# Optimization experiments

Hardware: AMD Instinct MI355X
Metric: run time of the kernel (lower is better)

## Reference

```python
import jax, jax.numpy as jnp
import numpy as np

F, C, H, W = 16, 256, 64, 64
N, M = 4096, 8192


def setup_inputs() -> dict:
    key = jax.random.key(0)
    k1, k2, k3, k4, k5 = jax.random.split(key, 5)
    proj_mats = jax.random.normal(k1, (F, 3, 3), dtype=jnp.float32)
    feats = jax.random.normal(k2, (F, C, H, W), dtype=jnp.float32)
    feat_img = jax.random.randint(k3, (N, 1), 0, F, dtype=jnp.int32)
    feat_loc = jax.random.uniform(k4, (N, 2), dtype=jnp.float32) * 64.0
    # tracks: [2, M] matched feature pairs, smaller index first (code contract).
    pair = jax.random.randint(k5, (2, M), 0, N, dtype=jnp.int32)
    tracks = jnp.sort(pair, axis=0)
    return {"proj_mats": proj_mats, "feats": feats, "feat_img": feat_img,
            "feat_loc": feat_loc, "tracks": tracks, "n_img": F}


def _association(tracks, n, n_img):
    """Faithful translation of find_3d_point_association +
    associate_3d_point_indices_2_features. The torch code raises a sparse
    symmetric adjacency (with identity diagonal) to the n_img-th power and
    uses only its NONZERO PATTERN. We use binary exponentiation with
    saturation (min(.,1)), which preserves the nonzero pattern exactly
    (all values are non-negative) while keeping values bounded."""
    A = jnp.zeros((n, n), dtype=jnp.float32)
    A = A.at[tracks[0], tracks[1]].set(1.0)
    A = A.at[tracks[1], tracks[0]].set(1.0)
    d = jnp.arange(n)
    A = A.at[d, d].set(1.0)  # identity diagonal, as in the torch code

    # T = pattern(A ** n_img) via binary exponentiation (n_img is a Python int)
    R, P, e = None, A, int(n_img)
    while e:
        if e & 1:
            R = P if R is None else jnp.minimum(R @ P, 1.0)
        e >>= 1
        if e:
            P = jnp.minimum(P @ P, 1.0)
    T = R

    # leading[j] = min{ i : T[i,j] != 0, i <= j }  (diag guarantees j itself)
    rows = d[:, None]
    cand = jnp.where((T > 0) & (rows <= d[None, :]), rows, n)
    leading = cand.min(axis=0)  # [N] int32

    # self-leading features get consecutive 3D-point ids in index order;
    # everyone else inherits the id of its (self-leading) leading feature.
    is_self = leading == d
    point_id = jnp.cumsum(is_self.astype(jnp.int32)) - 1  # rank among self-leading
    association = point_id[leading]
    return association


def reference(proj_mats, feats, feat_img, feat_loc, tracks, n_img):
    n = feat_img.shape[0]
    association = _association(tracks, n, n_img)
    return association
```

## Files before the change

kernel.cpp:

```cpp
#include <hip/hip_runtime.h>

#define NTHREADS 1024
#define MAXN 4096
#define EPT 8
#define NWAVES (NTHREADS / 64)

__global__ __launch_bounds__(NTHREADS) void ba_assoc_kernel(
    const int* __restrict__ tracks,
    int* __restrict__ out,
    int N, int M)
{
    const int tid  = threadIdx.x;
    const int lane = tid & 63;
    const int wid  = tid >> 6;

    __shared__ int lab[MAXN];
    __shared__ int pid[MAXN];
    __shared__ int wsum[NWAVES];
    __shared__ int chg;

    int eu[EPT], ev[EPT];
#pragma unroll
    for (int k = 0; k < EPT; ++k) {
        int e = tid + k * NTHREADS;
        if (e < M) { eu[k] = tracks[e]; ev[k] = tracks[M + e]; }
        else       { eu[k] = 0;         ev[k] = 0;             }
    }

    for (int i = tid; i < N; i += NTHREADS) lab[i] = i;
    __syncthreads();

    for (int it = 0; it < 64; ++it) {
        if (tid == 0) chg = 0;
        __syncthreads();

        int any = 0;
#pragma unroll
        for (int k = 0; k < EPT; ++k) {
            int u = eu[k], v = ev[k];
            int lu = lab[u];
            int lv = lab[v];
            if (lv < lu)      { int o = atomicMin(&lab[u], lv); any |= (o > lv); }
            else if (lu < lv) { int o = atomicMin(&lab[v], lu); any |= (o > lu); }
        }
        if (any) chg = 1;
        __syncthreads();
        if (!chg) break;

        for (int i = tid; i < N; i += NTHREADS) {
            int l = lab[i];
            int m = lab[l];
            if (m < l) atomicMin(&lab[i], m);
        }
        __syncthreads();
    }

    const int base = tid * 4;
    int f[4], s = 0;
#pragma unroll
    for (int k = 0; k < 4; ++k) {
        int idx = base + k;
        int fl = (idx < N && lab[idx] == idx) ? 1 : 0;
        f[k] = fl;
        s += fl;
    }
    int ps = s;
#pragma unroll
    for (int off = 1; off < 64; off <<= 1) {
        int t = __shfl_up(ps, off, 64);
        if (lane >= off) ps += t;
    }
    if (lane == 63) wsum[wid] = ps;
    __syncthreads();
    int wpre = 0;
    for (int w = 0; w < wid; ++w) wpre += wsum[w];
    int run = wpre + ps - s;

#pragma unroll
    for (int k = 0; k < 4; ++k) {
        int idx = base + k;
        run += f[k];
        if (idx < N) pid[idx] = run - 1;
    }
    __syncthreads();

    for (int i = tid; i < N; i += NTHREADS) out[i] = pid[lab[i]];
}

extern "C" void kernel_launch(void* const* d_in, const int* in_sizes, int n_in,
                              void* d_out, int out_size, void* d_ws, size_t ws_size,
                              hipStream_t stream) {
    const int* tracks = (const int*)d_in[4];
    int* out = (int*)d_out;
    const int N = in_sizes[2];
    const int M = in_sizes[4] / 2;
    ba_assoc_kernel<<<1, NTHREADS, 0, stream>>>(tracks, out, N, M);
}
```

Before: 17.88 us.

## Replace iterative label propagation with concurrent union-find in shared memory

Swaps the iterative min-label propagation with pointer jumping, which needed repeated barriers and convergence checks, for a single-pass concurrent union-find. It uses path halving and atomicCAS linking of the higher root to the lower root. Roots are then found read-only, and the shared parent array is reused to hold point ids. The goal is to avoid many synchronized iterations. In exchange, find loops are data-dependent and CAS retries can diverge, and the in-place path halving must stay correct under concurrent writes.

```diff
diff --git a/kernel.cpp b/kernel.cpp
--- a/kernel.cpp
+++ b/kernel.cpp
@@ -4,6 +4,24 @@
 #define MAXN 4096
 #define EPT 8
 #define NWAVES (NTHREADS / 64)
+
+
+__device__ __forceinline__ int find_halve(int* p, int x) {
+    int px = p[x];
+    while (px != x) {
+        int gp = p[px];
+        p[x] = gp;
+        x = gp;
+        px = p[x];
+    }
+    return x;
+}
+
+__device__ __forceinline__ int find_ro(const int* p, int x) {
+    int px = p[x];
+    while (px != x) { x = px; px = p[x]; }
+    return x;
+}
 
 __global__ __launch_bounds__(NTHREADS) void ba_assoc_kernel(
     const int* __restrict__ tracks,
@@ -14,10 +32,8 @@
     const int lane = tid & 63;
     const int wid  = tid >> 6;
 
-    __shared__ int lab[MAXN];
-    __shared__ int pid[MAXN];
+    __shared__ int par[MAXN];
     __shared__ int wsum[NWAVES];
-    __shared__ int chg;
 
     int eu[EPT], ev[EPT];
 #pragma unroll
@@ -27,43 +43,35 @@
         else       { eu[k] = 0;         ev[k] = 0;             }
     }
 
-    for (int i = tid; i < N; i += NTHREADS) lab[i] = i;
+    for (int i = tid; i < N; i += NTHREADS) par[i] = i;
     __syncthreads();
 
-    for (int it = 0; it < 64; ++it) {
-        if (tid == 0) chg = 0;
-        __syncthreads();
-
-        int any = 0;
 #pragma unroll
-        for (int k = 0; k < EPT; ++k) {
-            int u = eu[k], v = ev[k];
-            int lu = lab[u];
-            int lv = lab[v];
-            if (lv < lu)      { int o = atomicMin(&lab[u], lv); any |= (o > lv); }
-            else if (lu < lv) { int o = atomicMin(&lab[v], lu); any |= (o > lu); }
+    for (int k = 0; k < EPT; ++k) {
+        int u = eu[k], v = ev[k];
+        while (true) {
+            u = find_halve(par, u);
+            v = find_halve(par, v);
+            if (u == v) break;
+            int lo = min(u, v), hi = max(u, v);
+            if (atomicCAS(&par[hi], hi, lo) == hi) break;
+            u = lo; v = hi;
         }
-        if (any) chg = 1;
-        __syncthreads();
-        if (!chg) break;
-
-        for (int i = tid; i < N; i += NTHREADS) {
-            int l = lab[i];
-            int m = lab[l];
-            if (m < l) atomicMin(&lab[i], m);
-        }
-        __syncthreads();
     }
+    __syncthreads();
 
     const int base = tid * 4;
-    int f[4], s = 0;
+    int lead[4], f[4], s = 0;
 #pragma unroll
     for (int k = 0; k < 4; ++k) {
         int idx = base + k;
-        int fl = (idx < N && lab[idx] == idx) ? 1 : 0;
+        int r = (idx < N) ? find_ro(par, idx) : 0;
+        lead[k] = r;
+        int fl = (idx < N && r == idx) ? 1 : 0;
         f[k] = fl;
         s += fl;
     }
+
     int ps = s;
 #pragma unroll
     for (int off = 1; off < 64; off <<= 1) {
@@ -76,15 +84,20 @@
     for (int w = 0; w < wid; ++w) wpre += wsum[w];
     int run = wpre + ps - s;
 
+    __syncthreads();
 #pragma unroll
     for (int k = 0; k < 4; ++k) {
         int idx = base + k;
         run += f[k];
-        if (idx < N) pid[idx] = run - 1;
+        if (idx < N) par[idx] = run - 1;
     }
     __syncthreads();
 
-    for (int i = tid; i < N; i += NTHREADS) out[i] = pid[lab[i]];
+#pragma unroll
+    for (int k = 0; k < 4; ++k) {
+        int idx = base + k;
+        if (idx < N) out[idx] = par[lead[k]];
+    }
 }
 
 extern "C" void kernel_launch(void* const* d_in, const int* in_sizes, int n_in,
```

New measurement: 17.59 us. No clear change (-1.6%).
